# Optimization experiments

Hardware: AMD Instinct MI355X
Metric: run time of the kernel (lower is better)

The kernel has to match this reference:

```python
import jax, jax.numpy as jnp
import numpy as np

B, T, I, H = 128, 2048, 64, 128


def setup_inputs() -> dict:
    key = jax.random.key(0)
    ks = jax.random.split(key, 7)
    return {
        "input_data": jax.random.normal(ks[0], (B, T, I), dtype=jnp.float32),
        "h0": jax.random.normal(ks[1], (B, H), dtype=jnp.float32),
        "c0": jax.random.normal(ks[2], (B, H), dtype=jnp.float32),
        "W_ih": jax.random.normal(ks[3], (4 * H, I), dtype=jnp.float32) * 0.05,
        "W_hh": jax.random.normal(ks[4], (4 * H, H), dtype=jnp.float32) * 0.05,
        "b_ih": jax.random.normal(ks[5], (4 * H,), dtype=jnp.float32) * 0.05,
        "b_hh": jax.random.normal(ks[6], (4 * H,), dtype=jnp.float32) * 0.05,
    }


def reference(input_data, h0, c0, W_ih, W_hh, b_ih, b_hh):
    # Precompute input projections for all timesteps: [B, T, 4H]
    x_proj = jnp.einsum('bti,gi->btg', input_data, W_ih) + b_ih + b_hh

    def step(carry, xg):
        h, c = carry                      # [B, H]
        gates = xg + h @ W_hh.T           # [B, 4H]
        i_g, f_g, g_g, o_g = jnp.split(gates, 4, axis=-1)  # PyTorch order i,f,g,o
        i_g = jax.nn.sigmoid(i_g)
        f_g = jax.nn.sigmoid(f_g)
        g_g = jnp.tanh(g_g)
        o_g = jax.nn.sigmoid(o_g)
        c_new = f_g * c + i_g * g_g
        h_new = o_g * jnp.tanh(c_new)
        return (h_new, c_new), h_new

    (h_last, c_last), hs = jax.lax.scan(step, (h0, c0), jnp.swapaxes(x_proj, 0, 1))
    input_encoded = jnp.swapaxes(hs, 0, 1)  # [B, T, H]
    return (h_last[None], input_encoded)
```

## Files before the change

### kernel.cpp

```cpp
#include <hip/hip_runtime.h>

#define BB 128
#define TT 2048
#define II 64
#define HH 128
#define GG 512
#define KK 192
#define KC 48

typedef _Float16 h2 __attribute__((ext_vector_type(2)));

__device__ __forceinline__ h2 mkh2(float a, float b) {
    h2 r; r.x = (_Float16)a; r.y = (_Float16)b; return r;
}

__device__ __forceinline__ h2 u2h(unsigned u) {
    return __builtin_bit_cast(h2, u);
}

__device__ __forceinline__ float fdot2f(h2 a, h2 b, float c) {
#if __has_builtin(__builtin_amdgcn_fdot2)
    return __builtin_amdgcn_fdot2(a, b, c, false);
#else
    return fmaf((float)a.y, (float)b.y, fmaf((float)a.x, (float)b.x, c));
#endif
}

__device__ __forceinline__ float rcp_fast(float x) {
    return __builtin_amdgcn_rcpf(x);
}

__device__ __forceinline__ float tanh_fast(float x) {
    return fmaf(rcp_fast(1.0f + __expf(-2.0f * x)), 2.0f, -1.0f);
}

__device__ __forceinline__ float sigmoid_fast(float x) {
    return rcp_fast(1.0f + __expf(-x));
}

template <int CTRL>
__device__ __forceinline__ float dppq(float x) {
#if __has_builtin(__builtin_amdgcn_update_dpp)
    int i = __builtin_bit_cast(int, x);
    int r = __builtin_amdgcn_update_dpp(i, i, CTRL, 0xF, 0xF, true);
    return __builtin_bit_cast(float, r);
#else
    return __shfl_xor(x, (CTRL == 177) ? 1 : (CTRL == 78) ? 2 : 3, 4);
#endif
}

__global__ __launch_bounds__(512, 2) void lstm_fused_kernel(
    const float* __restrict__ input,
    const float* __restrict__ h0,
    const float* __restrict__ c0,
    const float* __restrict__ W_ih,
    const float* __restrict__ W_hh,
    const float* __restrict__ b_ih,
    const float* __restrict__ b_hh,
    float* __restrict__ out)
{
    __shared__ __align__(16) h2 s_xh[2][KK / 2];

    const int tid  = threadIdx.x;
    const int b    = blockIdx.x;
    const int lane = tid & 63;
    const int w    = tid >> 6;
    const int kc   = lane & 3;
    const int j    = (w << 4) | (lane >> 2);

    h2 wreg[4][KC / 2];
    float bias[4];
#pragma unroll
    for (int g = 0; g < 4; ++g) {
        const int row = (g << 7) | j;
        bias[g] = b_ih[row] + b_hh[row];
        const float2* wi = reinterpret_cast<const float2*>(W_ih + row * II);
        const float2* wh = reinterpret_cast<const float2*>(W_hh + row * HH);
#pragma unroll
        for (int m = 0; m < KC / 2; ++m) {
            const int k = KC * kc + 2 * m;
            float2 v = (k < II) ? wi[k >> 1] : wh[(k - II) >> 1];
            wreg[g][m] = mkh2(v.x, v.y);
        }
    }

    float c = c0[(size_t)b * HH + j];
    if (tid < 64) {
        float2 hv = reinterpret_cast<const float2*>(h0 + (size_t)b * HH)[tid];
        s_xh[0][32 + tid] = mkh2(hv.x, hv.y);
    }

    const float2* xin = reinterpret_cast<const float2*>(input) + (size_t)b * TT * 32 + tid;
    float2 xb0, xb1, xb2, xb3;
    if (tid < 32) {
        xb0 = xin[(size_t)0 * 32];
        xb1 = xin[(size_t)1 * 32];
        xb2 = xin[(size_t)2 * 32];
        xb3 = xin[(size_t)3 * 32];
        s_xh[0][tid] = mkh2(xb0.x, xb0.y);
        xb0 = xin[(size_t)4 * 32];
    }
    __syncthreads();

    float* out_h = out;
    float* out_e = out + BB * HH;
    float hlast = 0.0f;

    auto step = [&](int t, float2& xbn) {
        const int cb = t & 1, nb = cb ^ 1;

        if (tid < 32) {
            s_xh[nb][tid] = mkh2(xbn.x, xbn.y);
            int tn = t + 5; if (tn > TT - 1) tn = TT - 1;
            xbn = xin[(size_t)tn * 32];
        }

        const uint4* basep = reinterpret_cast<const uint4*>(
            reinterpret_cast<const char*>(s_xh[cb]) + kc * (KC * 2));

        float p0 = 0.0f, p1 = 0.0f, p2 = 0.0f, p3 = 0.0f;
#pragma unroll
        for (int q = 0; q < 6; ++q) {
            uint4 v = basep[q];
            p0 = fdot2f(wreg[0][4 * q + 0], u2h(v.x), p0);
            p1 = fdot2f(wreg[1][4 * q + 0], u2h(v.x), p1);
            p2 = fdot2f(wreg[2][4 * q + 0], u2h(v.x), p2);
            p3 = fdot2f(wreg[3][4 * q + 0], u2h(v.x), p3);
            p0 = fdot2f(wreg[0][4 * q + 1], u2h(v.y), p0);
            p1 = fdot2f(wreg[1][4 * q + 1], u2h(v.y), p1);
            p2 = fdot2f(wreg[2][4 * q + 1], u2h(v.y), p2);
            p3 = fdot2f(wreg[3][4 * q + 1], u2h(v.y), p3);
            p0 = fdot2f(wreg[0][4 * q + 2], u2h(v.z), p0);
            p1 = fdot2f(wreg[1][4 * q + 2], u2h(v.z), p1);
            p2 = fdot2f(wreg[2][4 * q + 2], u2h(v.z), p2);
            p3 = fdot2f(wreg[3][4 * q + 2], u2h(v.z), p3);
            p0 = fdot2f(wreg[0][4 * q + 3], u2h(v.w), p0);
            p1 = fdot2f(wreg[1][4 * q + 3], u2h(v.w), p1);
            p2 = fdot2f(wreg[2][4 * q + 3], u2h(v.w), p2);
            p3 = fdot2f(wreg[3][4 * q + 3], u2h(v.w), p3);
        }

        float u0 = p0 + dppq<177>(p0);
        float u1 = p1 + dppq<177>(p1);
        float u2 = p2 + dppq<177>(p2);
        float u3 = p3 + dppq<177>(p3);
        u0 += dppq<78>(u0);
        u1 += dppq<78>(u1);
        u2 += dppq<78>(u2);
        u3 += dppq<78>(u3);

        float ig = sigmoid_fast(u0 + bias[0]);
        float fg = sigmoid_fast(u1 + bias[1]);
        float gg = tanh_fast(u2 + bias[2]);
        float og = sigmoid_fast(u3 + bias[3]);

        c = fmaf(fg, c, ig * gg);
        float hv = og * tanh_fast(c);
        hlast = hv;

        if (kc == 0) reinterpret_cast<_Float16*>(s_xh[nb])[II + j] = (_Float16)hv;
        if (kc == 1) out_e[((size_t)b * TT + t) * HH + j] = hv;

        __syncthreads();
    };

    for (int t0 = 0; t0 < TT; t0 += 4) {
        step(t0 + 0, xb1);
        step(t0 + 1, xb2);
        step(t0 + 2, xb3);
        step(t0 + 3, xb0);
    }

    if (kc == 2) out_h[(size_t)b * HH + j] = hlast;
}

extern "C" void kernel_launch(void* const* d_in, const int* in_sizes, int n_in,
                              void* d_out, int out_size, void* d_ws, size_t ws_size,
                              hipStream_t stream) {
    const float* input = (const float*)d_in[0];
    const float* h0    = (const float*)d_in[1];
    const float* c0    = (const float*)d_in[2];
    const float* W_ih  = (const float*)d_in[3];
    const float* W_hh  = (const float*)d_in[4];
    const float* b_ih  = (const float*)d_in[5];
    const float* b_hh  = (const float*)d_in[6];
    float* out = (float*)d_out;

    hipLaunchKernelGGL(lstm_fused_kernel, dim3(BB), dim3(GG), 0, stream,
                       input, h0, c0, W_ih, W_hh, b_ih, b_hh, out);
}
```

Before: 1.572 ms.

## Process two batch rows per block to reuse register-resident weights

Each block now handles two batch elements instead of one, so the fp16 weights held in registers are reused for two dot products per step and the grid halves to 64 blocks. Per-step work per thread doubles, but the number of blocks and the per-block barrier overhead per batch row fall. The cost is a longer serial chain per step and only 64 of the many CUs in use, which may stretch the latency-bound recurrence.

```diff
diff --git a/kernel.cpp b/kernel.cpp
--- a/kernel.cpp
+++ b/kernel.cpp
@@ -4,9 +4,9 @@
 #define TT 2048
 #define II 64
 #define HH 128
-#define GG 512
 #define KK 192
 #define KC 48
+#define NB 2
 
 typedef _Float16 h2 __attribute__((ext_vector_type(2)));
 
@@ -59,10 +59,10 @@
     const float* __restrict__ b_hh,
     float* __restrict__ out)
 {
-    __shared__ __align__(16) h2 s_xh[2][KK / 2];
+    __shared__ __align__(16) h2 s_xh[2][NB][KK / 2];
 
     const int tid  = threadIdx.x;
-    const int b    = blockIdx.x;
+    const int b0   = blockIdx.x * NB;
     const int lane = tid & 63;
     const int w    = tid >> 6;
     const int kc   = lane & 3;
@@ -84,82 +84,94 @@
         }
     }
 
-    float c = c0[(size_t)b * HH + j];
+    float cc0 = c0[(size_t)(b0 + 0) * HH + j];
+    float cc1 = c0[(size_t)(b0 + 1) * HH + j];
+    if (tid < 128) {
+        const int bb = tid >> 6, i = tid & 63;
+        float2 hv = reinterpret_cast<const float2*>(h0 + (size_t)(b0 + bb) * HH)[i];
+        s_xh[0][bb][32 + i] = mkh2(hv.x, hv.y);
+    }
+
+    const int bbx = (tid >> 5) & 1, ix = tid & 31;
+    const float2* xin = reinterpret_cast<const float2*>(input)
+                        + (size_t)(b0 + bbx) * TT * 32 + ix;
+    float2 xb0, xb1, xb2, xb3;
     if (tid < 64) {
-        float2 hv = reinterpret_cast<const float2*>(h0 + (size_t)b * HH)[tid];
-        s_xh[0][32 + tid] = mkh2(hv.x, hv.y);
-    }
-
-    const float2* xin = reinterpret_cast<const float2*>(input) + (size_t)b * TT * 32 + tid;
-    float2 xb0, xb1, xb2, xb3;
-    if (tid < 32) {
         xb0 = xin[(size_t)0 * 32];
         xb1 = xin[(size_t)1 * 32];
         xb2 = xin[(size_t)2 * 32];
         xb3 = xin[(size_t)3 * 32];
-        s_xh[0][tid] = mkh2(xb0.x, xb0.y);
+        s_xh[0][bbx][ix] = mkh2(xb0.x, xb0.y);
         xb0 = xin[(size_t)4 * 32];
     }
     __syncthreads();
 
     float* out_h = out;
     float* out_e = out + BB * HH;
-    float hlast = 0.0f;
+    float hlast0 = 0.0f, hlast1 = 0.0f;
 
     auto step = [&](int t, float2& xbn) {
         const int cb = t & 1, nb = cb ^ 1;
 
-        if (tid < 32) {
-            s_xh[nb][tid] = mkh2(xbn.x, xbn.y);
+        if (tid < 64) {
+            s_xh[nb][bbx][ix] = mkh2(xbn.x, xbn.y);
             int tn = t + 5; if (tn > TT - 1) tn = TT - 1;
             xbn = xin[(size_t)tn * 32];
         }
 
-        const uint4* basep = reinterpret_cast<const uint4*>(
-            reinterpret_cast<const char*>(s_xh[cb]) + kc * (KC * 2));
-
-        float p0 = 0.0f, p1 = 0.0f, p2 = 0.0f, p3 = 0.0f;
+        const uint4* p0 = reinterpret_cast<const uint4*>(
+            reinterpret_cast<const char*>(s_xh[cb][0]) + kc * (KC * 2));
+        const uint4* p1 = reinterpret_cast<const uint4*>(
+            reinterpret_cast<const char*>(s_xh[cb][1]) + kc * (KC * 2));
+
+        float a0[4] = {0.f, 0.f, 0.f, 0.f};
+        float a1[4] = {0.f, 0.f, 0.f, 0.f};
 #pragma unroll
         for (int q = 0; q < 6; ++q) {
-            uint4 v = basep[q];
-            p0 = fdot2f(wreg[0][4 * q + 0], u2h(v.x), p0);
-            p1 = fdot2f(wreg[1][4 * q + 0], u2h(v.x), p1);
-            p2 = fdot2f(wreg[2][4 * q + 0], u2h(v.x), p2);
-            p3 = fdot2f(wreg[3][4 * q + 0], u2h(v.x), p3);
-            p0 = fdot2f(wreg[0][4 * q + 1], u2h(v.y), p0);
-            p1 = fdot2f(wreg[1][4 * q + 1], u2h(v.y), p1);
-            p2 = fdot2f(wreg[2][4 * q + 1], u2h(v.y), p2);
-            p3 = fdot2f(wreg[3][4 * q + 1], u2h(v.y), p3);
-            p0 = fdot2f(wreg[0][4 * q + 2], u2h(v.z), p0);
-            p1 = fdot2f(wreg[1][4 * q + 2], u2h(v.z), p1);
-            p2 = fdot2f(wreg[2][4 * q + 2], u2h(v.z), p2);
-            p3 = fdot2f(wreg[3][4 * q + 2], u2h(v.z), p3);
-            p0 = fdot2f(wreg[0][4 * q + 3], u2h(v.w), p0);
-            p1 = fdot2f(wreg[1][4 * q + 3], u2h(v.w), p1);
-            p2 = fdot2f(wreg[2][4 * q + 3], u2h(v.w), p2);
-            p3 = fdot2f(wreg[3][4 * q + 3], u2h(v.w), p3);
-        }
-
-        float u0 = p0 + dppq<177>(p0);
-        float u1 = p1 + dppq<177>(p1);
-        float u2 = p2 + dppq<177>(p2);
-        float u3 = p3 + dppq<177>(p3);
-        u0 += dppq<78>(u0);
-        u1 += dppq<78>(u1);
-        u2 += dppq<78>(u2);
-        u3 += dppq<78>(u3);
-
-        float ig = sigmoid_fast(u0 + bias[0]);
-        float fg = sigmoid_fast(u1 + bias[1]);
-        float gg = tanh_fast(u2 + bias[2]);
-        float og = sigmoid_fast(u3 + bias[3]);
-
-        c = fmaf(fg, c, ig * gg);
-        float hv = og * tanh_fast(c);
-        hlast = hv;
-
-        if (kc == 0) reinterpret_cast<_Float16*>(s_xh[nb])[II + j] = (_Float16)hv;
-        if (kc == 1) out_e[((size_t)b * TT + t) * HH + j] = hv;
+            uint4 v0 = p0[q];
+            uint4 v1 = p1[q];
+#pragma unroll
+            for (int g = 0; g < 4; ++g) {
+                a0[g] = fdot2f(wreg[g][4 * q + 0], u2h(v0.x), a0[g]);
+                a1[g] = fdot2f(wreg[g][4 * q + 0], u2h(v1.x), a1[g]);
+                a0[g] = fdot2f(wreg[g][4 * q + 1], u2h(v0.y), a0[g]);
+                a1[g] = fdot2f(wreg[g][4 * q + 1], u2h(v1.y), a1[g]);
+                a0[g] = fdot2f(wreg[g][4 * q + 2], u2h(v0.z), a0[g]);
+                a1[g] = fdot2f(wreg[g][4 * q + 2], u2h(v1.z), a1[g]);
+                a0[g] = fdot2f(wreg[g][4 * q + 3], u2h(v0.w), a0[g]);
+                a1[g] = fdot2f(wreg[g][4 * q + 3], u2h(v1.w), a1[g]);
+            }
+        }
+
+        float u0[4], u1[4];
+#pragma unroll
+        for (int g = 0; g < 4; ++g) {
+            float t0 = a0[g] + dppq<177>(a0[g]);
+            float t1 = a1[g] + dppq<177>(a1[g]);
+            u0[g] = t0 + dppq<78>(t0);
+            u1[g] = t1 + dppq<78>(t1);
+        }
+
+        float i0 = sigmoid_fast(u0[0] + bias[0]);
+        float i1 = sigmoid_fast(u1[0] + bias[0]);
+        float f0 = sigmoid_fast(u0[1] + bias[1]);
+        float f1 = sigmoid_fast(u1[1] + bias[1]);
+        float g0 = tanh_fast(u0[2] + bias[2]);
+        float g1 = tanh_fast(u1[2] + bias[2]);
+        float o0 = sigmoid_fast(u0[3] + bias[3]);
+        float o1 = sigmoid_fast(u1[3] + bias[3]);
+
+        cc0 = fmaf(f0, cc0, i0 * g0);
+        cc1 = fmaf(f1, cc1, i1 * g1);
+        float hv0 = o0 * tanh_fast(cc0);
+        float hv1 = o1 * tanh_fast(cc1);
+        hlast0 = hv0;
+        hlast1 = hv1;
+
+        if (kc == 0) reinterpret_cast<_Float16*>(s_xh[nb][0])[II + j] = (_Float16)hv0;
+        if (kc == 1) reinterpret_cast<_Float16*>(s_xh[nb][1])[II + j] = (_Float16)hv1;
+        if (kc == 2) out_e[((size_t)(b0 + 0) * TT + t) * HH + j] = hv0;
+        if (kc == 3) out_e[((size_t)(b0 + 1) * TT + t) * HH + j] = hv1;
 
         __syncthreads();
     };
@@ -171,7 +183,8 @@
         step(t0 + 3, xb0);
     }
 
-    if (kc == 2) out_h[(size_t)b * HH + j] = hlast;
+    if (kc == 0) out_h[(size_t)(b0 + 0) * HH + j] = hlast0;
+    if (kc == 1) out_h[(size_t)(b0 + 1) * HH + j] = hlast1;
 }
 
 extern "C" void kernel_launch(void* const* d_in, const int* in_sizes, int n_in,
@@ -186,6 +199,6 @@
     const float* b_hh  = (const float*)d_in[6];
     float* out = (float*)d_out;
 
-    hipLaunchKernelGGL(lstm_fused_kernel, dim3(BB), dim3(GG), 0, stream,
+    hipLaunchKernelGGL(lstm_fused_kernel, dim3(BB / NB), dim3(512), 0, stream,
                        input, h0, c0, W_ih, W_hh, b_ih, b_hh, out);
 }
```

After: 2.769 ms. +76.1%, slower.

## Replace per-step fdot2 gate matvec with MFMA 16x16x32 f16 instructions

Applied to the files above, without the earlier changes.

Each wave now computes its 16 hidden units' four gate pre-activations with MFMA 16x16x32 f16 ops, using weight fragments held in registers and the broadcast x/h vector as the B operand. Bias is folded into the accumulator init. The DPP cross-lane reductions are removed, and each lane selects its accumulator element directly. The aim is to shorten the serial per-timestep matvec latency, but most of the MFMA output columns are redundant because batch is 1 per block, and MFMA latency may dominate.

```diff
diff --git a/kernel.cpp b/kernel.cpp
--- a/kernel.cpp
+++ b/kernel.cpp
@@ -4,26 +4,14 @@
 #define TT 2048
 #define II 64
 #define HH 128
-#define GG 512
 #define KK 192
-#define KC 48
 
 typedef _Float16 h2 __attribute__((ext_vector_type(2)));
+typedef _Float16 f16x8 __attribute__((ext_vector_type(8)));
+typedef float f32x4 __attribute__((ext_vector_type(4)));
 
 __device__ __forceinline__ h2 mkh2(float a, float b) {
     h2 r; r.x = (_Float16)a; r.y = (_Float16)b; return r;
-}
-
-__device__ __forceinline__ h2 u2h(unsigned u) {
-    return __builtin_bit_cast(h2, u);
-}
-
-__device__ __forceinline__ float fdot2f(h2 a, h2 b, float c) {
-#if __has_builtin(__builtin_amdgcn_fdot2)
-    return __builtin_amdgcn_fdot2(a, b, c, false);
-#else
-    return fmaf((float)a.y, (float)b.y, fmaf((float)a.x, (float)b.x, c));
-#endif
 }
 
 __device__ __forceinline__ float rcp_fast(float x) {
@@ -36,17 +24,6 @@
 
 __device__ __forceinline__ float sigmoid_fast(float x) {
     return rcp_fast(1.0f + __expf(-x));
-}
-
-template <int CTRL>
-__device__ __forceinline__ float dppq(float x) {
-#if __has_builtin(__builtin_amdgcn_update_dpp)
-    int i = __builtin_bit_cast(int, x);
-    int r = __builtin_amdgcn_update_dpp(i, i, CTRL, 0xF, 0xF, true);
-    return __builtin_bit_cast(float, r);
-#else
-    return __shfl_xor(x, (CTRL == 177) ? 1 : (CTRL == 78) ? 2 : 3, 4);
-#endif
 }
 
 __global__ __launch_bounds__(512, 2) void lstm_fused_kernel(
@@ -65,26 +42,43 @@
     const int b    = blockIdx.x;
     const int lane = tid & 63;
     const int w    = tid >> 6;
-    const int kc   = lane & 3;
-    const int j    = (w << 4) | (lane >> 2);
+    const int grp  = lane >> 4;
+    const int m    = lane & 15;
+    const int r    = lane & 3;
+    const int jb   = (w << 4) | (grp << 2);
+    const int jown = jb | r;
 
-    h2 wreg[4][KC / 2];
-    float bias[4];
+    f16x8 wf[4][6];
 #pragma unroll
     for (int g = 0; g < 4; ++g) {
-        const int row = (g << 7) | j;
-        bias[g] = b_ih[row] + b_hh[row];
-        const float2* wi = reinterpret_cast<const float2*>(W_ih + row * II);
-        const float2* wh = reinterpret_cast<const float2*>(W_hh + row * HH);
+        const int row = (g << 7) | (w << 4) | m;
 #pragma unroll
-        for (int m = 0; m < KC / 2; ++m) {
-            const int k = KC * kc + 2 * m;
-            float2 v = (k < II) ? wi[k >> 1] : wh[(k - II) >> 1];
-            wreg[g][m] = mkh2(v.x, v.y);
+        for (int kt = 0; kt < 6; ++kt) {
+            const int k0 = 32 * kt + 8 * grp;
+            const float* src = (k0 < II) ? (W_ih + row * II + k0)
+                                         : (W_hh + row * HH + (k0 - II));
+            const float4 v0 = reinterpret_cast<const float4*>(src)[0];
+            const float4 v1 = reinterpret_cast<const float4*>(src)[1];
+            f16x8 f;
+            f[0] = (_Float16)v0.x; f[1] = (_Float16)v0.y;
+            f[2] = (_Float16)v0.z; f[3] = (_Float16)v0.w;
+            f[4] = (_Float16)v1.x; f[5] = (_Float16)v1.y;
+            f[6] = (_Float16)v1.z; f[7] = (_Float16)v1.w;
+            wf[g][kt] = f;
         }
     }
 
-    float c = c0[(size_t)b * HH + j];
+    f32x4 biasf[4];
+#pragma unroll
+    for (int g = 0; g < 4; ++g) {
+#pragma unroll
+        for (int rr = 0; rr < 4; ++rr) {
+            const int row = (g << 7) | (jb + rr);
+            biasf[g][rr] = b_ih[row] + b_hh[row];
+        }
+    }
+
+    float c = c0[(size_t)b * HH + jown];
     if (tid < 64) {
         float2 hv = reinterpret_cast<const float2*>(h0 + (size_t)b * HH)[tid];
         s_xh[0][32 + tid] = mkh2(hv.x, hv.y);
@@ -105,6 +99,7 @@
     float* out_h = out;
     float* out_e = out + BB * HH;
     float hlast = 0.0f;
+    const bool writer = (lane & 12) == 0;
 
     auto step = [&](int t, float2& xbn) {
         const int cb = t & 1, nb = cb ^ 1;
@@ -115,51 +110,41 @@
             xbn = xin[(size_t)tn * 32];
         }
 
-        const uint4* basep = reinterpret_cast<const uint4*>(
-            reinterpret_cast<const char*>(s_xh[cb]) + kc * (KC * 2));
+        const char* base = reinterpret_cast<const char*>(s_xh[cb]) + 16 * grp;
+        f16x8 bf[6];
+#pragma unroll
+        for (int kt = 0; kt < 6; ++kt)
+            bf[kt] = __builtin_bit_cast(f16x8,
+                *reinterpret_cast<const uint4*>(base + 64 * kt));
 
-        float p0 = 0.0f, p1 = 0.0f, p2 = 0.0f, p3 = 0.0f;
+        f32x4 acc0 = biasf[0], acc1 = biasf[1], acc2 = biasf[2], acc3 = biasf[3];
 #pragma unroll
-        for (int q = 0; q < 6; ++q) {
-            uint4 v = basep[q];
-            p0 = fdot2f(wreg[0][4 * q + 0], u2h(v.x), p0);
-            p1 = fdot2f(wreg[1][4 * q + 0], u2h(v.x), p1);
-            p2 = fdot2f(wreg[2][4 * q + 0], u2h(v.x), p2);
-            p3 = fdot2f(wreg[3][4 * q + 0], u2h(v.x), p3);
-            p0 = fdot2f(wreg[0][4 * q + 1], u2h(v.y), p0);
-            p1 = fdot2f(wreg[1][4 * q + 1], u2h(v.y), p1);
-            p2 = fdot2f(wreg[2][4 * q + 1], u2h(v.y), p2);
-            p3 = fdot2f(wreg[3][4 * q + 1], u2h(v.y), p3);
-            p0 = fdot2f(wreg[0][4 * q + 2], u2h(v.z), p0);
-            p1 = fdot2f(wreg[1][4 * q + 2], u2h(v.z), p1);
-            p2 = fdot2f(wreg[2][4 * q + 2], u2h(v.z), p2);
-            p3 = fdot2f(wreg[3][4 * q + 2], u2h(v.z), p3);
-            p0 = fdot2f(wreg[0][4 * q + 3], u2h(v.w), p0);
-            p1 = fdot2f(wreg[1][4 * q + 3], u2h(v.w), p1);
-            p2 = fdot2f(wreg[2][4 * q + 3], u2h(v.w), p2);
-            p3 = fdot2f(wreg[3][4 * q + 3], u2h(v.w), p3);
+        for (int kt = 0; kt < 6; ++kt) {
+            acc0 = __builtin_amdgcn_mfma_f32_16x16x32_f16(wf[0][kt], bf[kt], acc0, 0, 0, 0);
+            acc1 = __builtin_amdgcn_mfma_f32_16x16x32_f16(wf[1][kt], bf[kt], acc1, 0, 0, 0);
+            acc2 = __builtin_amdgcn_mfma_f32_16x16x32_f16(wf[2][kt], bf[kt], acc2, 0, 0, 0);
+            acc3 = __builtin_amdgcn_mfma_f32_16x16x32_f16(wf[3][kt], bf[kt], acc3, 0, 0, 0);
         }
 
-        float u0 = p0 + dppq<177>(p0);
-        float u1 = p1 + dppq<177>(p1);
-        float u2 = p2 + dppq<177>(p2);
-        float u3 = p3 + dppq<177>(p3);
-        u0 += dppq<78>(u0);
-        u1 += dppq<78>(u1);
-        u2 += dppq<78>(u2);
-        u3 += dppq<78>(u3);
+        const bool s1 = (lane & 1) != 0, s2 = (lane & 2) != 0;
+        float p0 = s2 ? (s1 ? acc0[3] : acc0[2]) : (s1 ? acc0[1] : acc0[0]);
+        float p1 = s2 ? (s1 ? acc1[3] : acc1[2]) : (s1 ? acc1[1] : acc1[0]);
+        float p2 = s2 ? (s1 ? acc2[3] : acc2[2]) : (s1 ? acc2[1] : acc2[0]);
+        float p3 = s2 ? (s1 ? acc3[3] : acc3[2]) : (s1 ? acc3[1] : acc3[0]);
 
-        float ig = sigmoid_fast(u0 + bias[0]);
-        float fg = sigmoid_fast(u1 + bias[1]);
-        float gg = tanh_fast(u2 + bias[2]);
-        float og = sigmoid_fast(u3 + bias[3]);
+        float ig = sigmoid_fast(p0);
+        float fg = sigmoid_fast(p1);
+        float gg = tanh_fast(p2);
+        float og = sigmoid_fast(p3);
 
         c = fmaf(fg, c, ig * gg);
         float hv = og * tanh_fast(c);
         hlast = hv;
 
-        if (kc == 0) reinterpret_cast<_Float16*>(s_xh[nb])[II + j] = (_Float16)hv;
-        if (kc == 1) out_e[((size_t)b * TT + t) * HH + j] = hv;
+        if (writer) {
+            reinterpret_cast<_Float16*>(s_xh[nb])[II + jown] = (_Float16)hv;
+            out_e[((size_t)b * TT + t) * HH + jown] = hv;
+        }
 
         __syncthreads();
     };
@@ -171,7 +156,7 @@
         step(t0 + 3, xb0);
     }
 
-    if (kc == 2) out_h[(size_t)b * HH + j] = hlast;
+    if (writer) out_h[(size_t)b * HH + jown] = hlast;
 }
 
 extern "C" void kernel_launch(void* const* d_in, const int* in_sizes, int n_in,
@@ -186,6 +171,6 @@
     const float* b_hh  = (const float*)d_in[6];
     float* out = (float*)d_out;
 
-    hipLaunchKernelGGL(lstm_fused_kernel, dim3(BB), dim3(GG), 0, stream,
+    hipLaunchKernelGGL(lstm_fused_kernel, dim3(BB), dim3(512), 0, stream,
                        input, h0, c0, W_ih, W_hh, b_ih, b_hh, out);
 }
```

Measured after the change: 1.293 ms. 17.8% less time.
